# Kernel tuning notes

Hardware: AMD Instinct MI355X
Metric: run time of the kernel (lower is better)

Reference implementation:

```python
import jax, jax.numpy as jnp
import numpy as np

PATCH = 32          # feature map is PATCH x PATCH, N = PATCH**2 tokens
HEADS = 8
HD = 24             # head_dim (hardcoded in Block -> Cluster3D)
P = 4               # proposal_w = proposal_h = 4 -> 16 cluster centers
EPS_NORM = 1e-12    # F.normalize eps
LN_EPS = 1e-5


def _layernorm(x, g, b):
    m = x.mean(-1, keepdims=True)
    v = ((x - m) ** 2).mean(-1, keepdims=True)
    return (x - m) / jnp.sqrt(v + LN_EPS) * g + b


def _cluster3d(xn, f_w, f_b, v_w, v_b, alpha, beta, proj_w, proj_b):
    # xn: [B, N, D] with tokens laid out row-major over a PATCH x PATCH grid
    B, N, D = xn.shape
    M = P * P
    feat = xn @ f_w.T + f_b   # [B, N, HEADS*HD]  (1x1 conv f)
    val = xn @ v_w.T + v_b    # [B, N, HEADS*HD]  (1x1 conv v)

    def to_heads(t):  # channel layout is (e c): head-major
        return t.reshape(B, N, HEADS, HD).transpose(0, 2, 1, 3).reshape(B * HEADS, N, HD)

    fh = to_heads(feat)       # [Bh, N, HD]
    vh = to_heads(val)

    def pool(t):  # AdaptiveAvgPool to (P, P) over the PATCH x PATCH grid
        g = t.reshape(-1, P, PATCH // P, P, PATCH // P, HD).mean(axis=(2, 4))
        return g.reshape(-1, M, HD)

    centers = pool(fh)        # [Bh, M, HD]
    vcenters = pool(vh)       # [Bh, M, HD]

    cn = centers / jnp.clip(jnp.linalg.norm(centers, axis=-1, keepdims=True), EPS_NORM)
    fn = fh / jnp.clip(jnp.linalg.norm(fh, axis=-1, keepdims=True), EPS_NORM)
    sim = beta + alpha * jnp.einsum('bmc,bnc->bmn', cn, fn)   # [Bh, M, N]
    sim = jnp.where(sim >= 0, sim, 0.2 * sim)                 # LeakyReLU(0.2); dropout eval=identity

    # hard top-1 assignment of each token to its best center
    idx = jnp.argmax(sim, axis=1)                              # [Bh, N]
    mask = jax.nn.one_hot(idx, M, dtype=sim.dtype).transpose(0, 2, 1)  # [Bh, M, N]
    mask = jax.lax.stop_gradient(mask)
    sim = sim * mask

    # aggregate tokens into centers, then dispatch back
    agg = (jnp.einsum('bmn,bnc->bmc', sim, vh) + vcenters) / (mask.sum(-1, keepdims=True) + 1.0)
    out = jnp.einsum('bmn,bmc->bnc', sim, agg)                 # [Bh, N, HD]

    out = out.reshape(B, HEADS, N, HD).transpose(0, 2, 1, 3).reshape(B, N, HEADS * HD)
    return out @ proj_w.T + proj_b                             # [B, N, D]


def setup_inputs() -> dict:
    key = jax.random.key(0)
    ks = jax.random.split(key, 8)
    B, N, D, HID, HH = 64, PATCH * PATCH, 512, 2048, HEADS * HD
    s = 0.02
    return {
        'x': jax.random.normal(ks[0], (B, N, D), jnp.float32),
        'ln1_g': jnp.ones((D,), jnp.float32),
        'ln1_b': jnp.zeros((D,), jnp.float32),
        'f_w': jax.random.normal(ks[1], (HH, D), jnp.float32) * s,
        'f_b': jnp.zeros((HH,), jnp.float32),
        'v_w': jax.random.normal(ks[2], (HH, D), jnp.float32) * s,
        'v_b': jnp.zeros((HH,), jnp.float32),
        'sim_alpha': jnp.ones((1,), jnp.float32),
        'sim_beta': jnp.zeros((1,), jnp.float32),
        'proj_w': jax.random.normal(ks[3], (D, HH), jnp.float32) * s,
        'proj_b': jnp.zeros((D,), jnp.float32),
        'ln2_g': jnp.ones((D,), jnp.float32),
        'ln2_b': jnp.zeros((D,), jnp.float32),
        'fc1_w': jax.random.normal(ks[4], (HID, D), jnp.float32) * s,
        'fc1_b': jnp.zeros((HID,), jnp.float32),
        'fc2_w': jax.random.normal(ks[5], (D, HID), jnp.float32) * s,
        'fc2_b': jnp.zeros((D,), jnp.float32),
    }


def reference(x, ln1_g, ln1_b, f_w, f_b, v_w, v_b, sim_alpha, sim_beta,
              proj_w, proj_b, ln2_g, ln2_b, fc1_w, fc1_b, fc2_w, fc2_b):
    x = x + _cluster3d(_layernorm(x, ln1_g, ln1_b), f_w, f_b, v_w, v_b,
                       sim_alpha, sim_beta, proj_w, proj_b)
    h = _layernorm(x, ln2_g, ln2_b)
    h = jax.nn.gelu(h @ fc1_w.T + fc1_b, approximate=False)
    x = x + (h @ fc2_w.T + fc2_b)
    return x
```

## Files before the change

### kernel.cpp

```cpp
#include <hip/hip_runtime.h>


typedef __attribute__((ext_vector_type(8))) short short8;
typedef __attribute__((ext_vector_type(4))) short short4v;
typedef __attribute__((ext_vector_type(4))) float floatx4;

static __device__ __forceinline__ short f2bf(float f) {
  union { float f; unsigned u; } a; a.f = f;
  unsigned r = a.u + 0x7fffu + ((a.u >> 16) & 1u);
  return (short)(r >> 16);
}

static __device__ __forceinline__ void gload_lds16(const short* g, short* l) {
  __builtin_amdgcn_global_load_lds(
      (const __attribute__((address_space(1))) void*)g,
      (__attribute__((address_space(3))) void*)l, 16, 0, 0);
}

__global__ __launch_bounds__(256) void cvt_f32_bf16(
    const float* __restrict__ in, short* __restrict__ out, int n4)
{
  int i = blockIdx.x * 256 + threadIdx.x;
  if (i >= n4) return;
  float4 v = reinterpret_cast<const float4*>(in)[i];
  short4v o;
  o[0] = f2bf(v.x); o[1] = f2bf(v.y); o[2] = f2bf(v.z); o[3] = f2bf(v.w);
  reinterpret_cast<short4v*>(out)[i] = o;
}

__global__ __launch_bounds__(256) void ln_kernel(
    const float* __restrict__ x, const float* __restrict__ g,
    const float* __restrict__ b, short* __restrict__ out)
{
  const int wave = threadIdx.x >> 6, lane = threadIdx.x & 63;
  const size_t row = (size_t)blockIdx.x * 4 + wave;
  const float* xr = x + row * 512;
  const int c = lane * 8;
  float4 v0 = *reinterpret_cast<const float4*>(xr + c);
  float4 v1 = *reinterpret_cast<const float4*>(xr + c + 4);
  float xs[8] = {v0.x, v0.y, v0.z, v0.w, v1.x, v1.y, v1.z, v1.w};
  float s = 0.f, q = 0.f;
#pragma unroll
  for (int k = 0; k < 8; ++k) { s += xs[k]; q += xs[k] * xs[k]; }
#pragma unroll
  for (int off = 32; off; off >>= 1) {
    s += __shfl_xor(s, off);
    q += __shfl_xor(q, off);
  }
  const float mean = s * (1.0f / 512.0f);
  const float var  = q * (1.0f / 512.0f) - mean * mean;
  const float rstd = rsqrtf(var + 1e-5f);
  short8 o;
#pragma unroll
  for (int k = 0; k < 8; ++k)
    o[k] = f2bf((xs[k] - mean) * rstd * g[c + k] + b[c + k]);
  *reinterpret_cast<short8*>(out + row * 512 + c) = o;
}

template<int BM, int BN, int WM, int WN, int EPI>
__global__ __launch_bounds__(256, 2) void gemm_bt(
    const short* __restrict__ A, const short* __restrict__ W,
    const float* __restrict__ bias, const float* __restrict__ resid,
    float* __restrict__ Cf, short* __restrict__ Cb,
    const int N, const int K)
{
  constexpr int BK = 32;
  constexpr int T  = 256;
  constexpr int AC = (BM * BK / 8) / T;
  constexpr int WC = (BN * BK / 8) / T;
  __shared__ short Al[2][BM * BK];
  __shared__ short Wl[2][BN * BK];
  const int tid  = threadIdx.x;
  const int wave = tid >> 6;
  const int lane = tid & 63;
  constexpr int WCOLS = BN / WN;
  const int wm = (wave / WCOLS) * WM;
  const int wn = (wave % WCOLS) * WN;
  constexpr int MI = WM / 16, NJ = WN / 16;
  const int row0 = blockIdx.x * BM;
  const int col0 = blockIdx.y * BN;
  const int r  = lane & 15;
  const int kc = lane >> 4;

  floatx4 acc[MI][NJ];
#pragma unroll
  for (int i = 0; i < MI; ++i)
#pragma unroll
    for (int j = 0; j < NJ; ++j)
      acc[i][j] = (floatx4){0.f, 0.f, 0.f, 0.f};

  const short* Ab = A + (size_t)row0 * K;
  const short* Wb = W + (size_t)col0 * K;

  const short* aSrc[AC]; int aDst[AC];
#pragma unroll
  for (int u = 0; u < AC; ++u) {
    const int cc = u * T + tid;
    const int rr = cc >> 2, sl = cc & 3;
    const int co = sl ^ ((rr >> 1) & 3);
    aSrc[u] = Ab + (size_t)rr * K + co * 8;
    aDst[u] = cc * 8;
  }
  const short* wSrc[WC]; int wDst[WC];
#pragma unroll
  for (int u = 0; u < WC; ++u) {
    const int cc = u * T + tid;
    const int rr = cc >> 2, sl = cc & 3;
    const int co = sl ^ ((rr >> 1) & 3);
    wSrc[u] = Wb + (size_t)rr * K + co * 8;
    wDst[u] = cc * 8;
  }
  int aOff[MI], wOff[NJ];
#pragma unroll
  for (int i = 0; i < MI; ++i) {
    const int rt = wm + 16 * i + r;
    aOff[i] = rt * BK + ((kc ^ ((rt >> 1) & 3)) << 3);
  }
#pragma unroll
  for (int j = 0; j < NJ; ++j) {
    const int rt = wn + 16 * j + r;
    wOff[j] = rt * BK + ((kc ^ ((rt >> 1) & 3)) << 3);
  }

  auto stage = [&](int buf, int k0) {
#pragma unroll
    for (int u = 0; u < AC; ++u) gload_lds16(aSrc[u] + k0, &Al[buf][aDst[u]]);
#pragma unroll
    for (int u = 0; u < WC; ++u) gload_lds16(wSrc[u] + k0, &Wl[buf][wDst[u]]);
  };

  stage(0, 0);
  __syncthreads();
  int cur = 0;
  for (int k0 = BK; k0 <= K; k0 += BK) {
    if (k0 < K) stage(cur ^ 1, k0);
    short8 af[MI], wfr[NJ];
#pragma unroll
    for (int i = 0; i < MI; ++i)
      af[i] = *reinterpret_cast<const short8*>(&Al[cur][aOff[i]]);
#pragma unroll
    for (int j = 0; j < NJ; ++j)
      wfr[j] = *reinterpret_cast<const short8*>(&Wl[cur][wOff[j]]);
#pragma unroll
    for (int i = 0; i < MI; ++i)
#pragma unroll
      for (int j = 0; j < NJ; ++j)
        acc[i][j] = __builtin_amdgcn_mfma_f32_16x16x32_bf16(
            af[i], wfr[j], acc[i][j], 0, 0, 0);
    __syncthreads();
    cur ^= 1;
  }

#pragma unroll
  for (int i = 0; i < MI; ++i) {
#pragma unroll
    for (int j = 0; j < NJ; ++j) {
      const int col = col0 + wn + 16 * j + r;
      const float bv = bias[col];
#pragma unroll
      for (int t = 0; t < 4; ++t) {
        const int rowi = row0 + wm + 16 * i + (lane >> 4) * 4 + t;
        const size_t offo = (size_t)rowi * N + col;
        float v = acc[i][j][t] + bv;
        if (EPI == 0) {
          Cf[offo] = v;
        } else if (EPI == 1) {
          Cf[offo] = v + resid[offo];
        } else {
          v = 0.5f * v * (1.0f + erff(v * 0.70710678118654752f));
          Cb[offo] = f2bf(v);
        }
      }
    }
  }
}

__global__ __launch_bounds__(384) void pool_kernel(
    const float* __restrict__ feat, const float* __restrict__ val,
    float* __restrict__ cn, float* __restrict__ vcent)
{
  const int bh = blockIdx.x;
  const int b = bh >> 3, h = bh & 7;
  const int t = threadIdx.x;
  const int m = t / 24, c = t % 24;
  const int cy = m >> 2, cx = m & 3;
  const size_t base = (size_t)b * 1024 * 192 + h * 24 + c;
  float sf = 0.f, sv = 0.f;
  for (int dy = 0; dy < 8; ++dy) {
    const int ny = (cy * 8 + dy) * 32 + cx * 8;
    for (int dx = 0; dx < 8; ++dx) {
      const size_t off = base + (size_t)(ny + dx) * 192;
      sf += feat[off];
      sv += val[off];
    }
  }
  sf *= (1.0f / 64.0f); sv *= (1.0f / 64.0f);
  __shared__ float cent[16][24];
  cent[m][c] = sf;
  vcent[(size_t)bh * 384 + t] = sv;
  __syncthreads();
  float nrm = 0.f;
#pragma unroll
  for (int k = 0; k < 24; ++k) nrm += cent[m][k] * cent[m][k];
  nrm = fmaxf(sqrtf(nrm), 1e-12f);
  cn[(size_t)bh * 384 + t] = sf / nrm;
}

__global__ __launch_bounds__(256) void sim_kernel(
    const float* __restrict__ feat, const float* __restrict__ cn,
    const float* __restrict__ alpha_p, const float* __restrict__ beta_p,
    float* __restrict__ sval, int* __restrict__ sidx)
{
  const int bh = blockIdx.y;
  const int b = bh >> 3, h = bh & 7;
  __shared__ float cs[384];
  for (int i = threadIdx.x; i < 384; i += 256) cs[i] = cn[(size_t)bh * 384 + i];
  __syncthreads();
  const int n = blockIdx.x * 256 + threadIdx.x;
  const float* f = feat + (size_t)(b * 1024 + n) * 192 + h * 24;
  float v[24];
#pragma unroll
  for (int k = 0; k < 24; k += 4) {
    float4 t4 = *reinterpret_cast<const float4*>(f + k);
    v[k] = t4.x; v[k + 1] = t4.y; v[k + 2] = t4.z; v[k + 3] = t4.w;
  }
  float q = 0.f;
#pragma unroll
  for (int k = 0; k < 24; ++k) q += v[k] * v[k];
  const float inv = 1.0f / fmaxf(sqrtf(q), 1e-12f);
  const float alpha = alpha_p[0], beta = beta_p[0];
  float best = -3.4e38f; int bi = 0;
#pragma unroll
  for (int m = 0; m < 16; ++m) {
    float d = 0.f;
#pragma unroll
    for (int k = 0; k < 24; ++k) d += cs[m * 24 + k] * v[k];
    float s = beta + alpha * (d * inv);
    s = (s < 0.f) ? 0.2f * s : s;
    if (s > best) { best = s; bi = m; }
  }
  sval[(size_t)bh * 1024 + n] = best;
  sidx[(size_t)bh * 1024 + n] = bi;
}

__global__ __launch_bounds__(256) void agg_kernel(
    const float* __restrict__ val, const float* __restrict__ vcent,
    const float* __restrict__ sval, const int* __restrict__ sidx,
    float* __restrict__ agg)
{
  const int bh = blockIdx.x;
  const int b = bh >> 3, h = bh & 7;
  __shared__ float acc[384];
  __shared__ float cnt[16];
  for (int i = threadIdx.x; i < 384; i += 256) acc[i] = 0.f;
  if (threadIdx.x < 16) cnt[threadIdx.x] = 0.f;
  __syncthreads();
  for (int n = threadIdx.x; n < 1024; n += 256) {
    const float s = sval[(size_t)bh * 1024 + n];
    const int m = sidx[(size_t)bh * 1024 + n];
    atomicAdd(&cnt[m], 1.0f);
    const float* vv = val + (size_t)(b * 1024 + n) * 192 + h * 24;
#pragma unroll
    for (int k = 0; k < 24; ++k) atomicAdd(&acc[m * 24 + k], s * vv[k]);
  }
  __syncthreads();
  for (int i = threadIdx.x; i < 384; i += 256) {
    const int m = i / 24;
    agg[(size_t)bh * 384 + i] = (acc[i] + vcent[(size_t)bh * 384 + i]) / (cnt[m] + 1.0f);
  }
}

__global__ __launch_bounds__(256) void dispatch_kernel(
    const float* __restrict__ sval, const int* __restrict__ sidx,
    const float* __restrict__ agg, short* __restrict__ o)
{
  const int g = blockIdx.x * 256 + threadIdx.x;
  const int h = g & 7, n = (g >> 3) & 1023, b = g >> 13;
  const int bh = b * 8 + h;
  const float s = sval[(size_t)bh * 1024 + n];
  const int m = sidx[(size_t)bh * 1024 + n];
  const float* a = agg + (size_t)bh * 384 + m * 24;
  short* op = o + ((size_t)(b * 1024 + n)) * 192 + h * 24;
  short8 pack[3];
#pragma unroll
  for (int k = 0; k < 24; ++k) pack[k >> 3][k & 7] = f2bf(s * a[k]);
  short8* dst = reinterpret_cast<short8*>(op);
  dst[0] = pack[0]; dst[1] = pack[1]; dst[2] = pack[2];
}

extern "C" void kernel_launch(void* const* d_in, const int* in_sizes, int n_in,
                              void* d_out, int out_size, void* d_ws, size_t ws_size,
                              hipStream_t stream)
{
  const float* x      = (const float*)d_in[0];
  const float* ln1_g  = (const float*)d_in[1];
  const float* ln1_b  = (const float*)d_in[2];
  const float* f_w    = (const float*)d_in[3];
  const float* f_b    = (const float*)d_in[4];
  const float* v_w    = (const float*)d_in[5];
  const float* v_b    = (const float*)d_in[6];
  const float* alpha  = (const float*)d_in[7];
  const float* beta   = (const float*)d_in[8];
  const float* proj_w = (const float*)d_in[9];
  const float* proj_b = (const float*)d_in[10];
  const float* ln2_g  = (const float*)d_in[11];
  const float* ln2_b  = (const float*)d_in[12];
  const float* fc1_w  = (const float*)d_in[13];
  const float* fc1_b  = (const float*)d_in[14];
  const float* fc2_w  = (const float*)d_in[15];
  const float* fc2_b  = (const float*)d_in[16];
  float* out = (float*)d_out;

  char* ws = (char*)d_ws;
  size_t off = 0;
  auto alloc = [&](size_t bytes) -> char* {
    char* p = ws + off;
    off = (off + bytes + 255) & ~(size_t)255;
    return p;
  };
  short* xn   = (short*)alloc(67108864);
  float* feat = (float*)alloc(50331648);
  float* val  = (float*)alloc(50331648);
  short* o    = (short*)alloc(25165824);
  float* x1   = (float*)alloc(134217728);
  short* wf   = (short*)alloc(196608);
  short* wv   = (short*)alloc(196608);
  short* wp   = (short*)alloc(196608);
  short* w1   = (short*)alloc(2097152);
  short* w2   = (short*)alloc(2097152);
  float* cnb  = (float*)alloc(786432);
  float* vcb  = (float*)alloc(786432);
  float* agb  = (float*)alloc(786432);
  float* svb  = (float*)alloc(2097152);
  int*   sib  = (int*)  alloc(2097152);
  short* h  = (short*)feat;
  short* h1 = xn;

  cvt_f32_bf16<<<96,   256, 0, stream>>>(f_w,    wf, 24576);
  cvt_f32_bf16<<<96,   256, 0, stream>>>(v_w,    wv, 24576);
  cvt_f32_bf16<<<96,   256, 0, stream>>>(proj_w, wp, 24576);
  cvt_f32_bf16<<<1024, 256, 0, stream>>>(fc1_w,  w1, 262144);
  cvt_f32_bf16<<<1024, 256, 0, stream>>>(fc2_w,  w2, 262144);

  ln_kernel<<<16384, 256, 0, stream>>>(x, ln1_g, ln1_b, xn);

  gemm_bt<256, 64, 64, 64, 0><<<dim3(256, 3), 256, 0, stream>>>(
      xn, wf, f_b, nullptr, feat, nullptr, 192, 512);
  gemm_bt<256, 64, 64, 64, 0><<<dim3(256, 3), 256, 0, stream>>>(
      xn, wv, v_b, nullptr, val, nullptr, 192, 512);

  pool_kernel<<<512, 384, 0, stream>>>(feat, val, cnb, vcb);
  sim_kernel<<<dim3(4, 512), 256, 0, stream>>>(feat, cnb, alpha, beta, svb, sib);
  agg_kernel<<<512, 256, 0, stream>>>(val, vcb, svb, sib, agb);
  dispatch_kernel<<<2048, 256, 0, stream>>>(svb, sib, agb, o);

  gemm_bt<128, 128, 64, 64, 1><<<dim3(512, 4), 256, 0, stream>>>(
      o, wp, proj_b, x, x1, nullptr, 512, 192);

  ln_kernel<<<16384, 256, 0, stream>>>(x1, ln2_g, ln2_b, h);

  for (int c = 0; c < 4; ++c) {
    const short* hA = h + (size_t)c * 16384 * 512;
    gemm_bt<128, 128, 64, 64, 2><<<dim3(128, 16), 256, 0, stream>>>(
        hA, w1, fc1_b, nullptr, nullptr, h1, 2048, 512);
    gemm_bt<128, 64, 64, 32, 1><<<dim3(128, 8), 256, 0, stream>>>(
        h1, w2, fc2_b, x1 + (size_t)c * 16384 * 512,
        out + (size_t)c * 16384 * 512, nullptr, 512, 2048);
  }
  (void)in_sizes; (void)n_in; (void)out_size; (void)ws_size;
}
```

Baseline: 1.002 ms.

## Use 256x256-tile 512-thread GEMM for MLP and enlarge chunk size

Adds a new gemm512 kernel with 256x256 block tiles, 8 waves of 128x64 warp tiles and BK=32 double-buffered LDS loads. It is used for the fc1 (GELU) and fc2 (residual) GEMMs in place of the smaller-tile gemm_bt. When enough workspace is available, it also allocates a dedicated h1 buffer so the MLP runs in 2 row chunks instead of 4. The larger tiles raise arithmetic intensity and cut launches, at the cost of heavy register use (launch bounds 512,1) and fewer blocks per chunk.

```diff
diff --git a/kernel.cpp b/kernel.cpp
--- a/kernel.cpp
+++ b/kernel.cpp
@@ -165,6 +165,122 @@
         if (EPI == 0) {
           Cf[offo] = v;
         } else if (EPI == 1) {
+          Cf[offo] = v + resid[offo];
+        } else {
+          v = 0.5f * v * (1.0f + erff(v * 0.70710678118654752f));
+          Cb[offo] = f2bf(v);
+        }
+      }
+    }
+  }
+}
+
+template<int EPI>
+__global__ __launch_bounds__(512, 1) void gemm512(
+    const short* __restrict__ A, const short* __restrict__ W,
+    const float* __restrict__ bias, const float* __restrict__ resid,
+    float* __restrict__ Cf, short* __restrict__ Cb,
+    const int N, const int K)
+{
+  constexpr int BM = 256, BN = 256, BK = 32;
+  constexpr int T  = 512;
+  constexpr int AC = (BM * BK / 8) / T;
+  constexpr int WC = (BN * BK / 8) / T;
+  constexpr int WM = 128, WN = 64;
+  constexpr int MI = WM / 16, NJ = WN / 16;
+  __shared__ short Al[2][BM * BK];
+  __shared__ short Wl[2][BN * BK];
+  const int tid  = threadIdx.x;
+  const int wave = tid >> 6;
+  const int lane = tid & 63;
+  const int wm = (wave >> 2) * WM;
+  const int wn = (wave & 3) * WN;
+  const int row0 = blockIdx.x * BM;
+  const int col0 = blockIdx.y * BN;
+  const int r  = lane & 15;
+  const int kc = lane >> 4;
+
+  floatx4 acc[MI][NJ];
+#pragma unroll
+  for (int i = 0; i < MI; ++i)
+#pragma unroll
+    for (int j = 0; j < NJ; ++j)
+      acc[i][j] = (floatx4){0.f, 0.f, 0.f, 0.f};
+
+  const short* Ab = A + (size_t)row0 * K;
+  const short* Wb = W + (size_t)col0 * K;
+
+  const short* aSrc[AC]; int aDst[AC];
+#pragma unroll
+  for (int u = 0; u < AC; ++u) {
+    const int cc = u * T + tid;
+    const int rr = cc >> 2, sl = cc & 3;
+    const int co = sl ^ ((rr >> 1) & 3);
+    aSrc[u] = Ab + (size_t)rr * K + co * 8;
+    aDst[u] = cc * 8;
+  }
+  const short* wSrc[WC]; int wDst[WC];
+#pragma unroll
+  for (int u = 0; u < WC; ++u) {
+    const int cc = u * T + tid;
+    const int rr = cc >> 2, sl = cc & 3;
+    const int co = sl ^ ((rr >> 1) & 3);
+    wSrc[u] = Wb + (size_t)rr * K + co * 8;
+    wDst[u] = cc * 8;
+  }
+  int aOff[MI], wOff[NJ];
+#pragma unroll
+  for (int i = 0; i < MI; ++i) {
+    const int rt = wm + 16 * i + r;
+    aOff[i] = rt * BK + ((kc ^ ((rt >> 1) & 3)) << 3);
+  }
+#pragma unroll
+  for (int j = 0; j < NJ; ++j) {
+    const int rt = wn + 16 * j + r;
+    wOff[j] = rt * BK + ((kc ^ ((rt >> 1) & 3)) << 3);
+  }
+
+  auto stage = [&](int buf, int k0) {
+#pragma unroll
+    for (int u = 0; u < AC; ++u) gload_lds16(aSrc[u] + k0, &Al[buf][aDst[u]]);
+#pragma unroll
+    for (int u = 0; u < WC; ++u) gload_lds16(wSrc[u] + k0, &Wl[buf][wDst[u]]);
+  };
+
+  stage(0, 0);
+  __syncthreads();
+  int cur = 0;
+  for (int k0 = BK; k0 <= K; k0 += BK) {
+    if (k0 < K) stage(cur ^ 1, k0);
+    short8 af[MI], wfr[NJ];
+#pragma unroll
+    for (int i = 0; i < MI; ++i)
+      af[i] = *reinterpret_cast<const short8*>(&Al[cur][aOff[i]]);
+#pragma unroll
+    for (int j = 0; j < NJ; ++j)
+      wfr[j] = *reinterpret_cast<const short8*>(&Wl[cur][wOff[j]]);
+#pragma unroll
+    for (int i = 0; i < MI; ++i)
+#pragma unroll
+      for (int j = 0; j < NJ; ++j)
+        acc[i][j] = __builtin_amdgcn_mfma_f32_16x16x32_bf16(
+            af[i], wfr[j], acc[i][j], 0, 0, 0);
+    __syncthreads();
+    cur ^= 1;
+  }
+
+#pragma unroll
+  for (int i = 0; i < MI; ++i) {
+#pragma unroll
+    for (int j = 0; j < NJ; ++j) {
+      const int col = col0 + wn + 16 * j + r;
+      const float bv = bias[col];
+#pragma unroll
+      for (int t = 0; t < 4; ++t) {
+        const int rowi = row0 + wm + 16 * i + kc * 4 + t;
+        const size_t offo = (size_t)rowi * N + col;
+        float v = acc[i][j][t] + bv;
+        if (EPI == 1) {
           Cf[offo] = v + resid[offo];
         } else {
           v = 0.5f * v * (1.0f + erff(v * 0.70710678118654752f));
@@ -334,7 +450,18 @@
   float* svb  = (float*)alloc(2097152);
   int*   sib  = (int*)  alloc(2097152);
   short* h  = (short*)feat;
-  short* h1 = xn;
+
+  const size_t h1_bytes = 134217728;
+  short* h1;
+  int nchunk;
+  if (ws_size >= off + h1_bytes) {
+    h1 = (short*)alloc(h1_bytes);
+    nchunk = 2;
+  } else {
+    h1 = xn;
+    nchunk = 4;
+  }
+  const int MCH = 65536 / nchunk;
 
   cvt_f32_bf16<<<96,   256, 0, stream>>>(f_w,    wf, 24576);
   cvt_f32_bf16<<<96,   256, 0, stream>>>(v_w,    wv, 24576);
@@ -359,13 +486,13 @@
 
   ln_kernel<<<16384, 256, 0, stream>>>(x1, ln2_g, ln2_b, h);
 
-  for (int c = 0; c < 4; ++c) {
-    const short* hA = h + (size_t)c * 16384 * 512;
-    gemm_bt<128, 128, 64, 64, 2><<<dim3(128, 16), 256, 0, stream>>>(
+  for (int c = 0; c < nchunk; ++c) {
+    const short* hA = h + (size_t)c * MCH * 512;
+    gemm512<2><<<dim3(MCH / 256, 8), 512, 0, stream>>>(
         hA, w1, fc1_b, nullptr, nullptr, h1, 2048, 512);
-    gemm_bt<128, 64, 64, 32, 1><<<dim3(128, 8), 256, 0, stream>>>(
-        h1, w2, fc2_b, x1 + (size_t)c * 16384 * 512,
-        out + (size_t)c * 16384 * 512, nullptr, 512, 2048);
-  }
-  (void)in_sizes; (void)n_in; (void)out_size; (void)ws_size;
-}
+    gemm512<1><<<dim3(MCH / 256, 2), 512, 0, stream>>>(
+        h1, w2, fc2_b, x1 + (size_t)c * MCH * 512,
+        out + (size_t)c * MCH * 512, nullptr, 512, 2048);
+  }
+  (void)in_sizes; (void)n_in; (void)out_size;
+}
```

New measurement: 1.184 ms. 18.1% more time.
